# Performance work log

Measured on AMD Instinct MI355X. Metric: run time of the kernel, lower is better.

The kernel has to match this reference:

```python
import jax, jax.numpy as jnp
import numpy as np
import math

NUM_HEADS = 8
DIM_EMBED = 640
DIM_CROSS = 768
DIM_HEAD = DIM_EMBED // NUM_HEADS


def setup_inputs() -> dict:
    key = jax.random.key(0)
    ks = jax.random.split(key, 10)
    B, SQ, SKV = 32, 1024, 77
    s_e = 1.0 / math.sqrt(DIM_EMBED)
    s_c = 1.0 / math.sqrt(DIM_CROSS)
    return {
        "x": jax.random.normal(ks[0], (B, SQ, DIM_EMBED), jnp.float32),
        "y": jax.random.normal(ks[1], (B, SKV, DIM_CROSS), jnp.float32),
        "Wq": jax.random.normal(ks[2], (DIM_EMBED, DIM_EMBED), jnp.float32) * s_e,
        "bq": jax.random.normal(ks[3], (DIM_EMBED,), jnp.float32) * 0.01,
        "Wk": jax.random.normal(ks[4], (DIM_CROSS, DIM_EMBED), jnp.float32) * s_c,
        "bk": jax.random.normal(ks[5], (DIM_EMBED,), jnp.float32) * 0.01,
        "Wv": jax.random.normal(ks[6], (DIM_CROSS, DIM_EMBED), jnp.float32) * s_c,
        "bv": jax.random.normal(ks[7], (DIM_EMBED,), jnp.float32) * 0.01,
        "Wo": jax.random.normal(ks[8], (DIM_EMBED, DIM_EMBED), jnp.float32) * s_e,
        "bo": jax.random.normal(ks[9], (DIM_EMBED,), jnp.float32) * 0.01,
    }


def reference(x, y, Wq, bq, Wk, bk, Wv, bv, Wo, bo):
    B, SQ, E = x.shape
    H, D = NUM_HEADS, DIM_HEAD
    q = x @ Wq + bq                      # [B, SQ, E]
    k = y @ Wk + bk                      # [B, SKV, E]
    v = y @ Wv + bv                      # [B, SKV, E]
    q = q.reshape(B, SQ, H, D)
    k = k.reshape(B, -1, H, D)
    v = v.reshape(B, -1, H, D)
    scores = jnp.einsum("bqhd,bkhd->bhqk", q, k) / math.sqrt(D)
    w = jax.nn.softmax(scores, axis=-1)
    out = jnp.einsum("bhqk,bkhd->bqhd", w, v).reshape(B, SQ, E)
    return out @ Wo + bo
```

## Files before the change

### kernel.cpp

```cpp
#include <hip/hip_runtime.h>
#include <hip/hip_bf16.h>

typedef __bf16 bf16x8 __attribute__((ext_vector_type(8)));
typedef float f32x4 __attribute__((ext_vector_type(4)));
typedef unsigned short us8 __attribute__((ext_vector_type(8)));

#define E_ 640
#define CD_ 768
#define B_ 32
#define SQ_ 1024
#define SKV_ 77
#define H_ 8
#define DH_ 80

typedef __attribute__((address_space(3))) unsigned int as3_u32;
typedef __attribute__((address_space(1))) const unsigned int as1_u32;

__device__ __forceinline__ void gload16(const unsigned short* g, unsigned short* l) {
    __builtin_amdgcn_global_load_lds((as1_u32*)g, (as3_u32*)l, 16, 0, 0);
}

__device__ __forceinline__ float b2f(unsigned short u) {
    unsigned int x = ((unsigned int)u) << 16;
    return __builtin_bit_cast(float, x);
}
__device__ __forceinline__ unsigned short f2b(float f) {
    unsigned int x = __builtin_bit_cast(unsigned int, f);
    x += 0x7fffu + ((x >> 16) & 1u);
    return (unsigned short)(x >> 16);
}
__device__ __forceinline__ bf16x8 lv8(const unsigned short* p) {
    return __builtin_bit_cast(bf16x8, *reinterpret_cast<const us8*>(p));
}
__device__ __forceinline__ bf16x8 zero8() {
    us8 z = {0,0,0,0,0,0,0,0};
    return __builtin_bit_cast(bf16x8, z);
}
__device__ __forceinline__ us8 cvt8(const float* s) {
    f32x4 f0 = *reinterpret_cast<const f32x4*>(s);
    f32x4 f1 = *reinterpret_cast<const f32x4*>(s + 4);
    us8 v;
    v[0]=f2b(f0[0]); v[1]=f2b(f0[1]); v[2]=f2b(f0[2]); v[3]=f2b(f0[3]);
    v[4]=f2b(f1[0]); v[5]=f2b(f1[1]); v[6]=f2b(f1[2]); v[7]=f2b(f1[3]);
    return v;
}

__device__ __forceinline__ void transpose_body(
    const float* __restrict__ in, unsigned short* __restrict__ out,
    int K, int N, int bx, int by, unsigned short (*t)[33])
{
    const int tx = threadIdx.x & 31, ty = threadIdx.x >> 5;
    const int n0 = bx * 32, k0 = by * 32;
#pragma unroll
    for (int i = 0; i < 4; ++i)
        t[ty + 8*i][tx] = f2b(in[(size_t)(k0 + ty + 8*i) * N + n0 + tx]);
    __syncthreads();
#pragma unroll
    for (int i = 0; i < 4; ++i)
        out[(size_t)(n0 + ty + 8*i) * K + k0 + tx] = t[tx][ty + 8*i];
}

__global__ __launch_bounds__(256) void fused_prep(
    const float* __restrict__ Wq, unsigned short* __restrict__ WqT,
    const float* __restrict__ Wo, unsigned short* __restrict__ WoT,
    const float* __restrict__ Wk, unsigned short* __restrict__ WkT,
    const float* __restrict__ Wv, unsigned short* __restrict__ WvT,
    const float* __restrict__ x, unsigned short* __restrict__ Xb)
{
    __shared__ unsigned short t[32][33];
    const int id = blockIdx.x;
    if (id < 800) {
        int z = id / 400, rem = id % 400;
        transpose_body(z ? Wo : Wq, z ? WoT : WqT, 640, 640, rem % 20, rem / 20, t);
    } else if (id < 1760) {
        int id2 = id - 800, z = id2 / 480, rem = id2 % 480;
        transpose_body(z ? Wv : Wk, z ? WvT : WkT, 768, 640, rem % 20, rem / 20, t);
    } else {
        long i = (long)(id - 1760) * 256 + threadIdx.x;
        const long stride = 2048L * 256;
        for (const long n8 = 2621440L; i < n8; i += stride)
            *reinterpret_cast<us8*>(Xb + i * 8) = cvt8(x + i * 8);
    }
}

template<int AMODE, bool CF32>
__device__ __forceinline__ void gemm_body(
    const void* __restrict__ Ap,
    const unsigned short* __restrict__ Wt,
    const float* __restrict__ bias,
    void* __restrict__ Cp,
    int M, int K, int ldc, int m0, int n0,
    unsigned short* smem)
{
    const int tid = threadIdx.x, lane = tid & 63, wave = tid >> 6;
    const int wr = (wave >> 1) << 6, wc = (wave & 1) << 6;
    const int l15 = lane & 15, l4 = lane >> 4;

    const int cw = wave * 64 + lane;
    const unsigned short* gW0 = Wt + (size_t)(n0 + (cw >> 2)) * K + (cw & 3) * 8;
    const unsigned short* gW1 = Wt + (size_t)(n0 + ((cw + 256) >> 2)) * K + ((cw + 256) & 3) * 8;

    const unsigned short* gA0; const unsigned short* gA1;
    const float* fA0; const float* fA1;
    if constexpr (AMODE == 0) {
        gA0 = (const unsigned short*)Ap + (size_t)(m0 + (cw >> 2)) * K + (cw & 3) * 8;
        gA1 = (const unsigned short*)Ap + (size_t)(m0 + ((cw + 256) >> 2)) * K + ((cw + 256) & 3) * 8;
    } else {
        int c0 = tid, c1 = tid + 256;
        int r0 = m0 + (c0 >> 2); if (r0 >= M) r0 = M - 1;
        int r1 = m0 + (c1 >> 2); if (r1 >= M) r1 = M - 1;
        fA0 = (const float*)Ap + (size_t)r0 * K + (c0 & 3) * 8;
        fA1 = (const float*)Ap + (size_t)r1 * K + (c1 & 3) * 8;
    }

    f32x4 acc[4][4];
#pragma unroll
    for (int m = 0; m < 4; ++m)
#pragma unroll
        for (int n = 0; n < 4; ++n)
#pragma unroll
            for (int i = 0; i < 4; ++i) acc[m][n][i] = 0.f;

    auto STAGE = [&](int buf) {
        unsigned short* As = smem + buf * 8192;
        unsigned short* Ws = As + 4096;
        if constexpr (AMODE == 0) {
            gload16(gA0, As + cw * 8);
            gload16(gA1, As + (cw + 256) * 8);
            gA0 += 32; gA1 += 32;
        } else {
            *reinterpret_cast<us8*>(As + tid * 8) = cvt8(fA0);
            *reinterpret_cast<us8*>(As + (tid + 256) * 8) = cvt8(fA1);
            fA0 += 32; fA1 += 32;
        }
        gload16(gW0, Ws + cw * 8);
        gload16(gW1, Ws + (cw + 256) * 8);
        gW0 += 32; gW1 += 32;
    };
    auto COMPUTE = [&](int buf) {
        const unsigned short* As = smem + buf * 8192;
        const unsigned short* Ws = As + 4096;
        bf16x8 a[4], b[4];
#pragma unroll
        for (int m = 0; m < 4; ++m)
            a[m] = lv8(&As[(wr + m * 16 + l15) * 32 + l4 * 8]);
#pragma unroll
        for (int n = 0; n < 4; ++n)
            b[n] = lv8(&Ws[(wc + n * 16 + l15) * 32 + l4 * 8]);
        __builtin_amdgcn_s_setprio(1);
#pragma unroll
        for (int m = 0; m < 4; ++m)
#pragma unroll
            for (int n = 0; n < 4; ++n)
                acc[m][n] = __builtin_amdgcn_mfma_f32_16x16x32_bf16(a[m], b[n], acc[m][n], 0, 0, 0);
        __builtin_amdgcn_s_setprio(0);
    };

    const int nk = K >> 5;
    STAGE(0);
    __syncthreads();
    for (int kt = 0; kt < nk - 2; kt += 2) {
        STAGE(1);
        COMPUTE(0);
        __syncthreads();
        STAGE(0);
        COMPUTE(1);
        __syncthreads();
    }
    STAGE(1);
    COMPUTE(0);
    __syncthreads();
    COMPUTE(1);

    float bs[4];
#pragma unroll
    for (int n = 0; n < 4; ++n) bs[n] = bias[n0 + wc + n * 16 + l15];

    if constexpr (CF32) {
        float* C = (float*)Cp;
        float* fs = (float*)smem;
#pragma unroll
        for (int p = 0; p < 2; ++p) {
            __syncthreads();
            if (wr == p * 64) {
#pragma unroll
                for (int m = 0; m < 4; ++m)
#pragma unroll
                    for (int n = 0; n < 4; ++n)
#pragma unroll
                        for (int i = 0; i < 4; ++i)
                            fs[(m * 16 + l4 * 4 + i) * 128 + wc + n * 16 + l15] =
                                acc[m][n][i] + bs[n];
            }
            __syncthreads();
#pragma unroll
            for (int r = 0; r < 8; ++r) {
                const int off = (r * 256 + tid) * 4;
                const int row = off >> 7, col = off & 127;
                const int grow = m0 + p * 64 + row;
                if (grow < M)
                    *reinterpret_cast<f32x4*>(&C[(size_t)grow * ldc + n0 + col]) =
                        *reinterpret_cast<const f32x4*>(&fs[off]);
            }
        }
    } else {
        unsigned short* C = (unsigned short*)Cp;
#pragma unroll
        for (int p = 0; p < 2; ++p) {
            __syncthreads();
            if (wr == p * 64) {
#pragma unroll
                for (int m = 0; m < 4; ++m)
#pragma unroll
                    for (int n = 0; n < 4; ++n)
#pragma unroll
                        for (int i = 0; i < 4; ++i)
                            smem[(m * 16 + l4 * 4 + i) * 128 + wc + n * 16 + l15] =
                                f2b(acc[m][n][i] + bs[n]);
            }
            __syncthreads();
#pragma unroll
            for (int r = 0; r < 4; ++r) {
                const int off = (r * 256 + tid) * 8;
                const int row = off >> 7, col = off & 127;
                const int grow = m0 + p * 64 + row;
                if (grow < M)
                    *reinterpret_cast<us8*>(&C[(size_t)grow * ldc + n0 + col]) =
                        *reinterpret_cast<us8*>(&smem[off]);
            }
        }
    }
}

__global__ __launch_bounds__(256) void gemm_o(
    const unsigned short* __restrict__ Ap, const unsigned short* __restrict__ Wt,
    const float* __restrict__ bias, float* __restrict__ Cp)
{
    __shared__ __align__(16) unsigned short smem[16384];
    const int orig = blockIdx.x;
    const int wgid = (orig & 7) * 160 + (orig >> 3);
    gemm_body<0, true>(Ap, Wt, bias, Cp, 32768, 640, 640, (wgid / 5) * 128, (wgid % 5) * 128, smem);
}

__global__ __launch_bounds__(256) void fused_qkv(
    const unsigned short* __restrict__ Xb, const unsigned short* __restrict__ WqT,
    const float* __restrict__ bq, unsigned short* __restrict__ Qb,
    const float* __restrict__ y,
    const unsigned short* __restrict__ WkT, const float* __restrict__ bk2, unsigned short* __restrict__ Kb,
    const unsigned short* __restrict__ WvT, const float* __restrict__ bv2, unsigned short* __restrict__ Vb)
{
    __shared__ __align__(16) unsigned short smem[16384];
    const int id = blockIdx.x;
    if (id < 200) {
        int z = id / 100, rem = id % 100;
        int m0 = (rem / 5) * 128, n0 = (rem % 5) * 128;
        if (z == 0) gemm_body<1, false>(y, WkT, bk2, Kb, 2464, 768, 640, m0, n0, smem);
        else        gemm_body<1, false>(y, WvT, bv2, Vb, 2464, 768, 640, m0, n0, smem);
    } else {
        int orig = id - 200;
        int wgid = (orig & 7) * 160 + (orig >> 3);
        int m0 = (wgid / 5) * 128, n0 = (wgid % 5) * 128;
        gemm_body<0, false>(Xb, WqT, bq, Qb, 32768, 640, 640, m0, n0, smem);
    }
}

__global__ __launch_bounds__(256) void vtrans_kernel(
    const unsigned short* __restrict__ Vb, unsigned short* __restrict__ Vt)
{
    __shared__ unsigned short Vl[77 * 88 + 8];
    const int b = blockIdx.x, h = blockIdx.y;
    const int tid = threadIdx.x;
    for (int idx = tid; idx < 770; idx += 256) {
        int kv = idx / 10, seg = idx % 10;
        *reinterpret_cast<us8*>(&Vl[kv * 88 + seg * 8]) =
            *reinterpret_cast<const us8*>(&Vb[(size_t)(b * 77 + kv) * 640 + h * 80 + seg * 8]);
    }
    __syncthreads();
    unsigned short* out = Vt + (size_t)(b * 8 + h) * 6400;
    for (int idx = tid; idx < 800; idx += 256) {
        int d = idx / 10, seg = idx % 10;
        us8 v;
#pragma unroll
        for (int j = 0; j < 8; ++j) {
            int kv = seg * 8 + j;
            v[j] = (kv < 77) ? Vl[kv * 88 + d] : (unsigned short)0;
        }
        *reinterpret_cast<us8*>(&out[d * 80 + seg * 8]) = v;
    }
}

__global__ __launch_bounds__(128) void attn_kernel(
    const unsigned short* __restrict__ Q,
    const unsigned short* __restrict__ Kp,
    const unsigned short* __restrict__ Vt,
    unsigned short* __restrict__ Oa)
{
    __shared__ __align__(16) unsigned short smem[11272];
    const int tid = threadIdx.x, lane = tid & 63, wave = tid >> 6;
    const int l15 = lane & 15, l4 = lane >> 4;
    const int qb = blockIdx.x * 128, h = blockIdx.y, b = blockIdx.z;
    const size_t qrow0 = (size_t)b * SQ_ + qb + wave * 64;
    const size_t kbase = (size_t)b * SKV_ * E_ + h * DH_;
    const size_t vbase = (size_t)(b * 8 + h) * 6400;

    bf16x8 aq[3][4];
#pragma unroll
    for (int ks = 0; ks < 3; ++ks) {
        const int d = ks * 32 + l4 * 8;
#pragma unroll
        for (int m = 0; m < 4; ++m)
            aq[ks][m] = (d < 80) ? lv8(&Q[(qrow0 + m * 16 + l15) * E_ + h * DH_ + d]) : zero8();
    }

    f32x4 accS[4][5];
#pragma unroll
    for (int m = 0; m < 4; ++m)
#pragma unroll
        for (int n = 0; n < 5; ++n)
#pragma unroll
            for (int i = 0; i < 4; ++i) accS[m][n][i] = 0.f;

#pragma unroll
    for (int ks = 0; ks < 3; ++ks) {
        const int d = ks * 32 + l4 * 8;
        bf16x8 bk[5];
#pragma unroll
        for (int n = 0; n < 5; ++n) {
            const int kv = n * 16 + l15;
            bk[n] = (kv < SKV_ && d < 80) ? lv8(&Kp[kbase + (size_t)kv * E_ + d]) : zero8();
        }
        __builtin_amdgcn_s_setprio(1);
#pragma unroll
        for (int n = 0; n < 5; ++n)
#pragma unroll
            for (int m = 0; m < 4; ++m)
                accS[m][n] = __builtin_amdgcn_mfma_f32_16x16x32_bf16(aq[ks][m], bk[n], accS[m][n], 0, 0, 0);
        __builtin_amdgcn_s_setprio(0);
    }

    unsigned short* Pw = smem + wave * 5632;

    const float scale = 0.11180339887498949f;
    float rs[4][4];
#pragma unroll
    for (int m = 0; m < 4; ++m) {
#pragma unroll
        for (int i = 0; i < 4; ++i) {
            float mx = -1e30f;
#pragma unroll
            for (int n = 0; n < 5; ++n) {
                float s = accS[m][n][i] * scale;
                if (n == 4 && l15 >= 13) s = -1e30f;
                accS[m][n][i] = s;
                mx = fmaxf(mx, s);
            }
            mx = fmaxf(mx, __shfl_xor(mx, 1));
            mx = fmaxf(mx, __shfl_xor(mx, 2));
            mx = fmaxf(mx, __shfl_xor(mx, 4));
            mx = fmaxf(mx, __shfl_xor(mx, 8));
            float sum = 0.f;
            const int prow = m * 16 + l4 * 4 + i;
#pragma unroll
            for (int n = 0; n < 5; ++n) {
                float p = __expf(accS[m][n][i] - mx);
                sum += p;
                Pw[prow * 88 + n * 16 + l15] = f2b(p);
            }
            sum += __shfl_xor(sum, 1);
            sum += __shfl_xor(sum, 2);
            sum += __shfl_xor(sum, 4);
            sum += __shfl_xor(sum, 8);
            rs[m][i] = sum;
        }
    }

    f32x4 accO[4][5];
#pragma unroll
    for (int m = 0; m < 4; ++m)
#pragma unroll
        for (int n = 0; n < 5; ++n)
#pragma unroll
            for (int i = 0; i < 4; ++i) accO[m][n][i] = 0.f;

#pragma unroll
    for (int ks = 0; ks < 3; ++ks) {
        const int kv = ks * 32 + l4 * 8;
        bf16x8 ap[4], bv[5];
#pragma unroll
        for (int m = 0; m < 4; ++m)
            ap[m] = (ks < 2 || l4 < 2) ? lv8(&Pw[(m * 16 + l15) * 88 + ks * 32 + l4 * 8])
                                       : zero8();
#pragma unroll
        for (int n = 0; n < 5; ++n) {
            const int d = n * 16 + l15;
            bv[n] = (kv < 80) ? lv8(&Vt[vbase + (size_t)d * 80 + kv]) : zero8();
        }
        __builtin_amdgcn_s_setprio(1);
#pragma unroll
        for (int n = 0; n < 5; ++n)
#pragma unroll
            for (int m = 0; m < 4; ++m)
                accO[m][n] = __builtin_amdgcn_mfma_f32_16x16x32_bf16(ap[m], bv[n], accO[m][n], 0, 0, 0);
        __builtin_amdgcn_s_setprio(0);
    }

    __syncthreads();
#pragma unroll
    for (int m = 0; m < 4; ++m) {
#pragma unroll
        for (int i = 0; i < 4; ++i) {
            const float inv = 1.f / rs[m][i];
            const int rl = wave * 64 + m * 16 + l4 * 4 + i;
#pragma unroll
            for (int n = 0; n < 5; ++n)
                smem[rl * 80 + n * 16 + l15] = f2b(accO[m][n][i] * inv);
        }
    }
    __syncthreads();
    const size_t obase = (size_t)b * SQ_ + qb;
    for (int idx = tid; idx < 1280; idx += 128) {
        int row = idx / 10, seg = idx % 10;
        *reinterpret_cast<us8*>(&Oa[(obase + row) * E_ + h * DH_ + seg * 8]) =
            *reinterpret_cast<us8*>(&smem[row * 80 + seg * 8]);
    }
}

extern "C" void kernel_launch(void* const* d_in, const int* in_sizes, int n_in,
                              void* d_out, int out_size, void* d_ws, size_t ws_size,
                              hipStream_t stream) {
    const float* x  = (const float*)d_in[0];
    const float* y  = (const float*)d_in[1];
    const float* Wq = (const float*)d_in[2];
    const float* bq = (const float*)d_in[3];
    const float* Wk = (const float*)d_in[4];
    const float* bk = (const float*)d_in[5];
    const float* Wv = (const float*)d_in[6];
    const float* bv = (const float*)d_in[7];
    const float* Wo = (const float*)d_in[8];
    const float* bo = (const float*)d_in[9];
    float* out = (float*)d_out;

    char* ws = (char*)d_ws;
    unsigned short* WqT = (unsigned short*)(ws + 0);
    unsigned short* WkT = (unsigned short*)(ws + 819200);
    unsigned short* WvT = (unsigned short*)(ws + 1802240);
    unsigned short* WoT = (unsigned short*)(ws + 2785280);
    unsigned short* Qb  = (unsigned short*)(ws + 3604480);
    unsigned short* Kb  = (unsigned short*)(ws + 45547520);
    unsigned short* Vb  = (unsigned short*)(ws + 48701440);
    unsigned short* Xb  = (unsigned short*)(ws + 51855360);
    unsigned short* Vtb = (unsigned short*)(ws + 51855360);

    fused_prep<<<3808, 256, 0, stream>>>(Wq, WqT, Wo, WoT, Wk, WkT, Wv, WvT, x, Xb);
    fused_qkv<<<1480, 256, 0, stream>>>(Xb, WqT, bq, Qb, y, WkT, bk, Kb, WvT, bv, Vb);
    vtrans_kernel<<<dim3(32, 8), 256, 0, stream>>>(Vb, Vtb);
    attn_kernel<<<dim3(8, 8, 32), 128, 0, stream>>>(Qb, Kb, Vtb, Qb);
    gemm_o<<<1280, 256, 0, stream>>>(Qb, WoT, bo, out);
}
```

Measured before the change: 174.5 us.

## Fuse x fp32-to-bf16 conversion into Q projection GEMM via LDS fp32 staging

Drops the separate pass that converts x to bf16 in the prep kernel. The Q GEMM now loads fp32 x tiles straight into LDS with async global_load_lds, using an XOR swizzle to avoid bank conflicts, and converts to bf16 with v_cvt_pk_bf16_f32 when forming MFMA operands. This removes a full write and re-read of the bf16 copy of x. In exchange, LDS use per block grows from 32KB to 48KB, which may reduce occupancy, and the Q tiles now read twice as many bytes.

```diff
diff --git a/kernel.cpp b/kernel.cpp
--- a/kernel.cpp
+++ b/kernel.cpp
@@ -4,6 +4,7 @@
 typedef __bf16 bf16x8 __attribute__((ext_vector_type(8)));
 typedef float f32x4 __attribute__((ext_vector_type(4)));
 typedef unsigned short us8 __attribute__((ext_vector_type(8)));
+typedef unsigned int u32x4 __attribute__((ext_vector_type(4)));
 
 #define E_ 640
 #define CD_ 768
@@ -19,6 +20,9 @@
 __device__ __forceinline__ void gload16(const unsigned short* g, unsigned short* l) {
     __builtin_amdgcn_global_load_lds((as1_u32*)g, (as3_u32*)l, 16, 0, 0);
 }
+__device__ __forceinline__ void gload16f(const float* g, unsigned short* l) {
+    __builtin_amdgcn_global_load_lds((as1_u32*)g, (as3_u32*)l, 16, 0, 0);
+}
 
 __device__ __forceinline__ float b2f(unsigned short u) {
     unsigned int x = ((unsigned int)u) << 16;
@@ -44,6 +48,15 @@
     v[4]=f2b(f1[0]); v[5]=f2b(f1[1]); v[6]=f2b(f1[2]); v[7]=f2b(f1[3]);
     return v;
 }
+__device__ __forceinline__ bf16x8 cvtpk8(f32x4 lo, f32x4 hi) {
+    unsigned int w0, w1, w2, w3;
+    asm("v_cvt_pk_bf16_f32 %0, %1, %2" : "=v"(w0) : "v"(lo[0]), "v"(lo[1]));
+    asm("v_cvt_pk_bf16_f32 %0, %1, %2" : "=v"(w1) : "v"(lo[2]), "v"(lo[3]));
+    asm("v_cvt_pk_bf16_f32 %0, %1, %2" : "=v"(w2) : "v"(hi[0]), "v"(hi[1]));
+    asm("v_cvt_pk_bf16_f32 %0, %1, %2" : "=v"(w3) : "v"(hi[2]), "v"(hi[3]));
+    u32x4 w = {w0, w1, w2, w3};
+    return __builtin_bit_cast(bf16x8, w);
+}
 
 __device__ __forceinline__ void transpose_body(
     const float* __restrict__ in, unsigned short* __restrict__ out,
@@ -64,22 +77,16 @@
     const float* __restrict__ Wq, unsigned short* __restrict__ WqT,
     const float* __restrict__ Wo, unsigned short* __restrict__ WoT,
     const float* __restrict__ Wk, unsigned short* __restrict__ WkT,
-    const float* __restrict__ Wv, unsigned short* __restrict__ WvT,
-    const float* __restrict__ x, unsigned short* __restrict__ Xb)
+    const float* __restrict__ Wv, unsigned short* __restrict__ WvT)
 {
     __shared__ unsigned short t[32][33];
     const int id = blockIdx.x;
     if (id < 800) {
         int z = id / 400, rem = id % 400;
         transpose_body(z ? Wo : Wq, z ? WoT : WqT, 640, 640, rem % 20, rem / 20, t);
-    } else if (id < 1760) {
+    } else {
         int id2 = id - 800, z = id2 / 480, rem = id2 % 480;
         transpose_body(z ? Wv : Wk, z ? WvT : WkT, 768, 640, rem % 20, rem / 20, t);
-    } else {
-        long i = (long)(id - 1760) * 256 + threadIdx.x;
-        const long stride = 2048L * 256;
-        for (const long n8 = 2621440L; i < n8; i += stride)
-            *reinterpret_cast<us8*>(Xb + i * 8) = cvt8(x + i * 8);
     }
 }
 
@@ -92,6 +99,8 @@
     int M, int K, int ldc, int m0, int n0,
     unsigned short* smem)
 {
+    constexpr int BUFSTRIDE = (AMODE == 2) ? 12288 : 8192;
+    constexpr int AWOFF     = (AMODE == 2) ? 8192 : 4096;
     const int tid = threadIdx.x, lane = tid & 63, wave = tid >> 6;
     const int wr = (wave >> 1) << 6, wc = (wave & 1) << 6;
     const int l15 = lane & 15, l4 = lane >> 4;
@@ -102,15 +111,24 @@
 
     const unsigned short* gA0; const unsigned short* gA1;
     const float* fA0; const float* fA1;
+    const float* xbase; int aoff[4];
     if constexpr (AMODE == 0) {
         gA0 = (const unsigned short*)Ap + (size_t)(m0 + (cw >> 2)) * K + (cw & 3) * 8;
         gA1 = (const unsigned short*)Ap + (size_t)(m0 + ((cw + 256) >> 2)) * K + ((cw + 256) & 3) * 8;
-    } else {
+    } else if constexpr (AMODE == 1) {
         int c0 = tid, c1 = tid + 256;
         int r0 = m0 + (c0 >> 2); if (r0 >= M) r0 = M - 1;
         int r1 = m0 + (c1 >> 2); if (r1 >= M) r1 = M - 1;
         fA0 = (const float*)Ap + (size_t)r0 * K + (c0 & 3) * 8;
         fA1 = (const float*)Ap + (size_t)r1 * K + (c1 & 3) * 8;
+    } else {
+        xbase = (const float*)Ap + (size_t)m0 * K;
+#pragma unroll
+        for (int j = 0; j < 4; ++j) {
+            int c = j * 256 + tid;
+            int row = c >> 3, sg = (c & 7) ^ (row & 7);
+            aoff[j] = row * K + sg * 4;
+        }
     }
 
     f32x4 acc[4][4];
@@ -122,28 +140,46 @@
             for (int i = 0; i < 4; ++i) acc[m][n][i] = 0.f;
 
     auto STAGE = [&](int buf) {
-        unsigned short* As = smem + buf * 8192;
-        unsigned short* Ws = As + 4096;
+        unsigned short* As = smem + buf * BUFSTRIDE;
+        unsigned short* Ws = As + AWOFF;
         if constexpr (AMODE == 0) {
             gload16(gA0, As + cw * 8);
             gload16(gA1, As + (cw + 256) * 8);
             gA0 += 32; gA1 += 32;
-        } else {
+        } else if constexpr (AMODE == 1) {
             *reinterpret_cast<us8*>(As + tid * 8) = cvt8(fA0);
             *reinterpret_cast<us8*>(As + (tid + 256) * 8) = cvt8(fA1);
             fA0 += 32; fA1 += 32;
+        } else {
+#pragma unroll
+            for (int j = 0; j < 4; ++j)
+                gload16f(xbase + aoff[j], As + (j * 256 + tid) * 8);
+            xbase += 32;
         }
         gload16(gW0, Ws + cw * 8);
         gload16(gW1, Ws + (cw + 256) * 8);
         gW0 += 32; gW1 += 32;
     };
     auto COMPUTE = [&](int buf) {
-        const unsigned short* As = smem + buf * 8192;
-        const unsigned short* Ws = As + 4096;
+        const unsigned short* As = smem + buf * BUFSTRIDE;
+        const unsigned short* Ws = As + AWOFF;
         bf16x8 a[4], b[4];
-#pragma unroll
-        for (int m = 0; m < 4; ++m)
-            a[m] = lv8(&As[(wr + m * 16 + l15) * 32 + l4 * 8]);
+        if constexpr (AMODE == 2) {
+            const float* Af = (const float*)As;
+#pragma unroll
+            for (int m = 0; m < 4; ++m) {
+                const int row = wr + m * 16 + l15;
+                const int t0 = (l4 * 2) ^ (row & 7);
+                const int t1 = (l4 * 2 + 1) ^ (row & 7);
+                f32x4 lo = *reinterpret_cast<const f32x4*>(Af + row * 32 + t0 * 4);
+                f32x4 hi = *reinterpret_cast<const f32x4*>(Af + row * 32 + t1 * 4);
+                a[m] = cvtpk8(lo, hi);
+            }
+        } else {
+#pragma unroll
+            for (int m = 0; m < 4; ++m)
+                a[m] = lv8(&As[(wr + m * 16 + l15) * 32 + l4 * 8]);
+        }
 #pragma unroll
         for (int n = 0; n < 4; ++n)
             b[n] = lv8(&Ws[(wc + n * 16 + l15) * 32 + l4 * 8]);
@@ -243,13 +279,13 @@
 }
 
 __global__ __launch_bounds__(256) void fused_qkv(
-    const unsigned short* __restrict__ Xb, const unsigned short* __restrict__ WqT,
+    const float* __restrict__ x, const unsigned short* __restrict__ WqT,
     const float* __restrict__ bq, unsigned short* __restrict__ Qb,
     const float* __restrict__ y,
     const unsigned short* __restrict__ WkT, const float* __restrict__ bk2, unsigned short* __restrict__ Kb,
     const unsigned short* __restrict__ WvT, const float* __restrict__ bv2, unsigned short* __restrict__ Vb)
 {
-    __shared__ __align__(16) unsigned short smem[16384];
+    __shared__ __align__(16) unsigned short smem[24576];
     const int id = blockIdx.x;
     if (id < 200) {
         int z = id / 100, rem = id % 100;
@@ -260,7 +296,7 @@
         int orig = id - 200;
         int wgid = (orig & 7) * 160 + (orig >> 3);
         int m0 = (wgid / 5) * 128, n0 = (wgid % 5) * 128;
-        gemm_body<0, false>(Xb, WqT, bq, Qb, 32768, 640, 640, m0, n0, smem);
+        gemm_body<2, false>(x, WqT, bq, Qb, 32768, 640, 640, m0, n0, smem);
     }
 }
 
@@ -448,11 +484,10 @@
     unsigned short* Qb  = (unsigned short*)(ws + 3604480);
     unsigned short* Kb  = (unsigned short*)(ws + 45547520);
     unsigned short* Vb  = (unsigned short*)(ws + 48701440);
-    unsigned short* Xb  = (unsigned short*)(ws + 51855360);
     unsigned short* Vtb = (unsigned short*)(ws + 51855360);
 
-    fused_prep<<<3808, 256, 0, stream>>>(Wq, WqT, Wo, WoT, Wk, WkT, Wv, WvT, x, Xb);
-    fused_qkv<<<1480, 256, 0, stream>>>(Xb, WqT, bq, Qb, y, WkT, bk, Kb, WvT, bv, Vb);
+    fused_prep<<<1760, 256, 0, stream>>>(Wq, WqT, Wo, WoT, Wk, WkT, Wv, WvT);
+    fused_qkv<<<1480, 256, 0, stream>>>(x, WqT, bq, Qb, y, WkT, bk, Kb, WvT, bv, Vb);
     vtrans_kernel<<<dim3(32, 8), 256, 0, stream>>>(Vb, Vtb);
     attn_kernel<<<dim3(8, 8, 32), 128, 0, stream>>>(Qb, Kb, Vtb, Qb);
     gemm_o<<<1280, 256, 0, stream>>>(Qb, WoT, bo, out);
```

Result: faster. 166.4 us (-4.7%).

## Fuse x fp32-to-bf16 conversion into Q GEMM, swizzle LDS, use packed cvt

Applied to the files above, without the earlier changes.

Drops the separate pass that converts x to bf16 in the prep kernel. The Q projection GEMM now reads fp32 x directly and converts it while staging into LDS, which removes a full write and re-read of the bf16 copy of x. The change also adds an XOR swizzle on the LDS tile layout to reduce bank conflicts on the MFMA operand reads, and replaces the manual rounding with the hardware v_cvt_pk_bf16_f32 instruction. In exchange, the Q GEMM loads twice the bytes for A and does the conversion through registers instead of using async global_load_lds, which may stall its pipeline.

```diff
diff --git a/kernel.cpp b/kernel.cpp
--- a/kernel.cpp
+++ b/kernel.cpp
@@ -4,6 +4,7 @@
 typedef __bf16 bf16x8 __attribute__((ext_vector_type(8)));
 typedef float f32x4 __attribute__((ext_vector_type(4)));
 typedef unsigned short us8 __attribute__((ext_vector_type(8)));
+typedef unsigned int u32x4 __attribute__((ext_vector_type(4)));
 
 #define E_ 640
 #define CD_ 768
@@ -36,13 +37,19 @@
     us8 z = {0,0,0,0,0,0,0,0};
     return __builtin_bit_cast(bf16x8, z);
 }
+__device__ __forceinline__ bf16x8 cvtpk8(f32x4 lo, f32x4 hi) {
+    unsigned int w0, w1, w2, w3;
+    asm("v_cvt_pk_bf16_f32 %0, %1, %2" : "=v"(w0) : "v"(lo[0]), "v"(lo[1]));
+    asm("v_cvt_pk_bf16_f32 %0, %1, %2" : "=v"(w1) : "v"(lo[2]), "v"(lo[3]));
+    asm("v_cvt_pk_bf16_f32 %0, %1, %2" : "=v"(w2) : "v"(hi[0]), "v"(hi[1]));
+    asm("v_cvt_pk_bf16_f32 %0, %1, %2" : "=v"(w3) : "v"(hi[2]), "v"(hi[3]));
+    u32x4 w = {w0, w1, w2, w3};
+    return __builtin_bit_cast(bf16x8, w);
+}
 __device__ __forceinline__ us8 cvt8(const float* s) {
     f32x4 f0 = *reinterpret_cast<const f32x4*>(s);
     f32x4 f1 = *reinterpret_cast<const f32x4*>(s + 4);
-    us8 v;
-    v[0]=f2b(f0[0]); v[1]=f2b(f0[1]); v[2]=f2b(f0[2]); v[3]=f2b(f0[3]);
-    v[4]=f2b(f1[0]); v[5]=f2b(f1[1]); v[6]=f2b(f1[2]); v[7]=f2b(f1[3]);
-    return v;
+    return __builtin_bit_cast(us8, cvtpk8(f0, f1));
 }
 
 __device__ __forceinline__ void transpose_body(
@@ -64,22 +71,16 @@
     const float* __restrict__ Wq, unsigned short* __restrict__ WqT,
     const float* __restrict__ Wo, unsigned short* __restrict__ WoT,
     const float* __restrict__ Wk, unsigned short* __restrict__ WkT,
-    const float* __restrict__ Wv, unsigned short* __restrict__ WvT,
-    const float* __restrict__ x, unsigned short* __restrict__ Xb)
+    const float* __restrict__ Wv, unsigned short* __restrict__ WvT)
 {
     __shared__ unsigned short t[32][33];
     const int id = blockIdx.x;
     if (id < 800) {
         int z = id / 400, rem = id % 400;
         transpose_body(z ? Wo : Wq, z ? WoT : WqT, 640, 640, rem % 20, rem / 20, t);
-    } else if (id < 1760) {
+    } else {
         int id2 = id - 800, z = id2 / 480, rem = id2 % 480;
         transpose_body(z ? Wv : Wk, z ? WvT : WkT, 768, 640, rem % 20, rem / 20, t);
-    } else {
-        long i = (long)(id - 1760) * 256 + threadIdx.x;
-        const long stride = 2048L * 256;
-        for (const long n8 = 2621440L; i < n8; i += stride)
-            *reinterpret_cast<us8*>(Xb + i * 8) = cvt8(x + i * 8);
     }
 }
 
@@ -95,22 +96,26 @@
     const int tid = threadIdx.x, lane = tid & 63, wave = tid >> 6;
     const int wr = (wave >> 1) << 6, wc = (wave & 1) << 6;
     const int l15 = lane & 15, l4 = lane >> 4;
-
-    const int cw = wave * 64 + lane;
-    const unsigned short* gW0 = Wt + (size_t)(n0 + (cw >> 2)) * K + (cw & 3) * 8;
-    const unsigned short* gW1 = Wt + (size_t)(n0 + ((cw + 256) >> 2)) * K + ((cw + 256) & 3) * 8;
+    const int sgz = (tid >> 3) & 3;
+    const int srd = (l15 >> 1) & 3;
+    const int rdo = (l4 ^ srd) << 3;
+
+    const unsigned short* gW0 = Wt + (size_t)(n0 + (tid >> 2)) * K + (((tid & 3) ^ sgz) << 3);
+    const unsigned short* gW1 = Wt + (size_t)(n0 + (tid >> 2) + 64) * K + (((tid & 3) ^ sgz) << 3);
 
     const unsigned short* gA0; const unsigned short* gA1;
     const float* fA0; const float* fA1;
+    int sw0, sw1;
     if constexpr (AMODE == 0) {
-        gA0 = (const unsigned short*)Ap + (size_t)(m0 + (cw >> 2)) * K + (cw & 3) * 8;
-        gA1 = (const unsigned short*)Ap + (size_t)(m0 + ((cw + 256) >> 2)) * K + ((cw + 256) & 3) * 8;
+        gA0 = (const unsigned short*)Ap + (size_t)(m0 + (tid >> 2)) * K + (((tid & 3) ^ sgz) << 3);
+        gA1 = (const unsigned short*)Ap + (size_t)(m0 + (tid >> 2) + 64) * K + (((tid & 3) ^ sgz) << 3);
     } else {
-        int c0 = tid, c1 = tid + 256;
-        int r0 = m0 + (c0 >> 2); if (r0 >= M) r0 = M - 1;
-        int r1 = m0 + (c1 >> 2); if (r1 >= M) r1 = M - 1;
-        fA0 = (const float*)Ap + (size_t)r0 * K + (c0 & 3) * 8;
-        fA1 = (const float*)Ap + (size_t)r1 * K + (c1 & 3) * 8;
+        int r0 = m0 + (tid >> 2); if (r0 >= M) r0 = M - 1;
+        int r1 = r0 + 64; if (r1 >= M) r1 = M - 1;
+        fA0 = (const float*)Ap + (size_t)r0 * K + (tid & 3) * 8;
+        fA1 = (const float*)Ap + (size_t)r1 * K + (tid & 3) * 8;
+        sw0 = ((tid & ~3) | ((tid & 3) ^ sgz)) * 8;
+        sw1 = sw0 + 256 * 8;
     }
 
     f32x4 acc[4][4];
@@ -125,16 +130,16 @@
         unsigned short* As = smem + buf * 8192;
         unsigned short* Ws = As + 4096;
         if constexpr (AMODE == 0) {
-            gload16(gA0, As + cw * 8);
-            gload16(gA1, As + (cw + 256) * 8);
+            gload16(gA0, As + tid * 8);
+            gload16(gA1, As + (tid + 256) * 8);
             gA0 += 32; gA1 += 32;
         } else {
-            *reinterpret_cast<us8*>(As + tid * 8) = cvt8(fA0);
-            *reinterpret_cast<us8*>(As + (tid + 256) * 8) = cvt8(fA1);
+            *reinterpret_cast<us8*>(As + sw0) = cvt8(fA0);
+            *reinterpret_cast<us8*>(As + sw1) = cvt8(fA1);
             fA0 += 32; fA1 += 32;
         }
-        gload16(gW0, Ws + cw * 8);
-        gload16(gW1, Ws + (cw + 256) * 8);
+        gload16(gW0, Ws + tid * 8);
+        gload16(gW1, Ws + (tid + 256) * 8);
         gW0 += 32; gW1 += 32;
     };
     auto COMPUTE = [&](int buf) {
@@ -143,10 +148,10 @@
         bf16x8 a[4], b[4];
 #pragma unroll
         for (int m = 0; m < 4; ++m)
-            a[m] = lv8(&As[(wr + m * 16 + l15) * 32 + l4 * 8]);
+            a[m] = lv8(&As[(wr + m * 16 + l15) * 32 + rdo]);
 #pragma unroll
         for (int n = 0; n < 4; ++n)
-            b[n] = lv8(&Ws[(wc + n * 16 + l15) * 32 + l4 * 8]);
+            b[n] = lv8(&Ws[(wc + n * 16 + l15) * 32 + rdo]);
         __builtin_amdgcn_s_setprio(1);
 #pragma unroll
         for (int m = 0; m < 4; ++m)
@@ -239,11 +244,12 @@
     __shared__ __align__(16) unsigned short smem[16384];
     const int orig = blockIdx.x;
     const int wgid = (orig & 7) * 160 + (orig >> 3);
-    gemm_body<0, true>(Ap, Wt, bias, Cp, 32768, 640, 640, (wgid / 5) * 128, (wgid % 5) * 128, smem);
+    gemm_body<0, true>(Ap, Wt, bias, Cp, 32768, 640, 640,
+                       (wgid / 5) * 128, (wgid % 5) * 128, smem);
 }
 
 __global__ __launch_bounds__(256) void fused_qkv(
-    const unsigned short* __restrict__ Xb, const unsigned short* __restrict__ WqT,
+    const float* __restrict__ x, const unsigned short* __restrict__ WqT,
     const float* __restrict__ bq, unsigned short* __restrict__ Qb,
     const float* __restrict__ y,
     const unsigned short* __restrict__ WkT, const float* __restrict__ bk2, unsigned short* __restrict__ Kb,
@@ -260,7 +266,7 @@
         int orig = id - 200;
         int wgid = (orig & 7) * 160 + (orig >> 3);
         int m0 = (wgid / 5) * 128, n0 = (wgid % 5) * 128;
-        gemm_body<0, false>(Xb, WqT, bq, Qb, 32768, 640, 640, m0, n0, smem);
+        gemm_body<1, false>(x, WqT, bq, Qb, 32768, 640, 640, m0, n0, smem);
     }
 }
 
@@ -448,11 +454,10 @@
     unsigned short* Qb  = (unsigned short*)(ws + 3604480);
     unsigned short* Kb  = (unsigned short*)(ws + 45547520);
     unsigned short* Vb  = (unsigned short*)(ws + 48701440);
-    unsigned short* Xb  = (unsigned short*)(ws + 51855360);
     unsigned short* Vtb = (unsigned short*)(ws + 51855360);
 
-    fused_prep<<<3808, 256, 0, stream>>>(Wq, WqT, Wo, WoT, Wk, WkT, Wv, WvT, x, Xb);
-    fused_qkv<<<1480, 256, 0, stream>>>(Xb, WqT, bq, Qb, y, WkT, bk, Kb, WvT, bv, Vb);
+    fused_prep<<<1760, 256, 0, stream>>>(Wq, WqT, Wo, WoT, Wk, WkT, Wv, WvT);
+    fused_qkv<<<1480, 256, 0, stream>>>(x, WqT, bq, Qb, y, WkT, bk, Kb, WvT, bv, Vb);
     vtrans_kernel<<<dim3(32, 8), 256, 0, stream>>>(Vb, Vtb);
     attn_kernel<<<dim3(8, 8, 32), 128, 0, stream>>>(Qb, Kb, Vtb, Qb);
     gemm_o<<<1280, 256, 0, stream>>>(Qb, WoT, bo, out);
```

Result: faster. 162.9 us (-6.7%).
